# Kernel optimization log

Measured on AMD Instinct MI355X. Metric: run time of the kernel, lower is better.

## Reference

```python
import jax, jax.numpy as jnp
import numpy as np


def _sage_layer(x, src, dst, W_self, W_neigh, b, n_nodes):
    # mean aggregation over incoming edges: agg[v] = mean(x[u] for (u,v) in E)
    agg = jax.ops.segment_sum(x[src], dst, num_segments=n_nodes)          # [N, D]
    cnt = jax.ops.segment_sum(jnp.ones((src.shape[0],), x.dtype), dst,
                              num_segments=n_nodes)                        # [N]
    agg = agg / jnp.clip(cnt, 1.0)[:, None]
    # h = ReLU(x W_self^T + agg W_neigh^T + b)   (torch Linear weight is [out, in])
    h = jnp.einsum('nd,od->no', x, W_self) + jnp.einsum('nd,od->no', agg, W_neigh) + b
    return jax.nn.relu(h)


def setup_inputs() -> dict:
    key = jax.random.key(0)
    ks = jax.random.split(key, 7)
    N, E = 50000, 800000
    F_IN, H, F_OUT = 128, 256, 128
    x = jax.random.normal(ks[0], (N, F_IN), dtype=jnp.float32)
    edge_index = jax.random.randint(ks[1], (2, E), 0, N, dtype=jnp.int64)
    s = 0.05
    return {
        'x': x,
        'edge_index': edge_index,
        'W_self1': jax.random.normal(ks[2], (H, F_IN), dtype=jnp.float32) * s,
        'W_neigh1': jax.random.normal(ks[3], (H, F_IN), dtype=jnp.float32) * s,
        'b1': jnp.zeros((H,), dtype=jnp.float32),
        'W_self2': jax.random.normal(ks[4], (F_OUT, H), dtype=jnp.float32) * s,
        'W_neigh2': jax.random.normal(ks[5], (F_OUT, H), dtype=jnp.float32) * s,
        'b2': jnp.zeros((F_OUT,), dtype=jnp.float32),
    }


def reference(x, edge_index, W_self1, W_neigh1, b1, W_self2, W_neigh2, b2):
    n_nodes = x.shape[0]
    src, dst = edge_index[0], edge_index[1]
    h = _sage_layer(x, src, dst, W_self1, W_neigh1, b1, n_nodes)
    # dropout is identity at inference
    h = _sage_layer(h, src, dst, W_self2, W_neigh2, b2, n_nodes)
    return h
```

## Files before the change

kernel.cpp:

```cpp
#include <hip/hip_runtime.h>


#define CAP 64
#define CPAD 16
#define NSLICE 8

typedef __attribute__((ext_vector_type(8))) short bfrag;
typedef __attribute__((ext_vector_type(4))) float ffrag;

__device__ inline unsigned short f2bf(float f) {
    union { float f; unsigned u; } v; v.f = f;
    unsigned r = (v.u + 0x7FFFu + ((v.u >> 16) & 1u)) >> 16;
    return (unsigned short)r;
}

__global__ __launch_bounds__(256) void prep_kernel(
        const int* __restrict__ src, const int* __restrict__ dst,
        int* __restrict__ cnt, unsigned short* __restrict__ adj,
        int E, int nper, int nfill,
        const float* __restrict__ x, unsigned short* __restrict__ xb, long xn4,
        int xblocks,
        const float* __restrict__ W0, const float* __restrict__ W1,
        const float* __restrict__ W2, const float* __restrict__ W3,
        unsigned short* __restrict__ O0, unsigned short* __restrict__ O1,
        unsigned short* __restrict__ O2, unsigned short* __restrict__ O3)
{
    int b = blockIdx.x;
    if (b < nfill) {
        int slice = b & (NSLICE - 1);
        int e = (b >> 3) * 256 + (int)threadIdx.x;
        if (e >= E) return;
        int d = dst[e];
        if ((unsigned)(d - slice * nper) >= (unsigned)nper) return;
        int r = atomicAdd(&cnt[d * CPAD], 1);
        if (r < CAP) adj[(size_t)d * CAP + r] = (unsigned short)src[e];
        return;
    }
    b -= nfill;
    if (b < xblocks) {
        long i = (long)b * 256 + threadIdx.x;
        if (i >= xn4) return;
        float4 v = *(const float4*)(x + i * 4);
        ushort4 o;
        o.x = f2bf(v.x); o.y = f2bf(v.y); o.z = f2bf(v.z); o.w = f2bf(v.w);
        *(ushort4*)(xb + i * 4) = o;
        return;
    }
    b -= xblocks;
    int i = b * 256 + (int)threadIdx.x;
    int sel = i >> 13, off = i & 8191;
    const float* srcw = (sel == 0) ? W0 : (sel == 1) ? W1 : (sel == 2) ? W2 : W3;
    unsigned short* dstw = (sel == 0) ? O0 : (sel == 1) ? O1 : (sel == 2) ? O2 : O3;
    float4 v = ((const float4*)srcw)[off];
    ushort4 o;
    o.x = f2bf(v.x); o.y = f2bf(v.y); o.z = f2bf(v.z); o.w = f2bf(v.w);
    ((ushort4*)dstw)[off] = o;
}

#define BFLO(u) __uint_as_float((u) << 16)
#define BFHI(u) __uint_as_float((u) & 0xFFFF0000u)

__global__ __launch_bounds__(256) void gather_mean_bf16(
        const unsigned short* __restrict__ Xb, const int* __restrict__ cnt,
        const unsigned short* __restrict__ adj,
        unsigned short* __restrict__ aggb, int N) {
    int w = (blockIdx.x * 256 + threadIdx.x) >> 6;
    int lane = threadIdx.x & 63;
    int node = w * 2 + (lane >> 5);
    int sl = lane & 31;
    if (node >= N) return;
    int c = cnt[node * CPAD]; if (c > CAP) c = CAP;
    const unsigned short* al = adj + (size_t)node * CAP;
    float a0 = 0.f, a1 = 0.f, a2 = 0.f, a3 = 0.f;
    int j = 0;
    for (; j + 3 < c; j += 4) {
        int s0 = al[j], s1 = al[j + 1], s2 = al[j + 2], s3 = al[j + 3];
        uint2 v0 = *(const uint2*)(Xb + (size_t)s0 * 128 + sl * 4);
        uint2 v1 = *(const uint2*)(Xb + (size_t)s1 * 128 + sl * 4);
        uint2 v2 = *(const uint2*)(Xb + (size_t)s2 * 128 + sl * 4);
        uint2 v3 = *(const uint2*)(Xb + (size_t)s3 * 128 + sl * 4);
        a0 += (BFLO(v0.x) + BFLO(v1.x)) + (BFLO(v2.x) + BFLO(v3.x));
        a1 += (BFHI(v0.x) + BFHI(v1.x)) + (BFHI(v2.x) + BFHI(v3.x));
        a2 += (BFLO(v0.y) + BFLO(v1.y)) + (BFLO(v2.y) + BFLO(v3.y));
        a3 += (BFHI(v0.y) + BFHI(v1.y)) + (BFHI(v2.y) + BFHI(v3.y));
    }
    for (; j < c; ++j) {
        uint2 v = *(const uint2*)(Xb + (size_t)al[j] * 128 + sl * 4);
        a0 += BFLO(v.x); a1 += BFHI(v.x);
        a2 += BFLO(v.y); a3 += BFHI(v.y);
    }
    float s = (c > 0) ? 1.0f / (float)c : 0.0f;
    uint2 o;
    o.x = (unsigned)f2bf(a0 * s) | ((unsigned)f2bf(a1 * s) << 16);
    o.y = (unsigned)f2bf(a2 * s) | ((unsigned)f2bf(a3 * s) << 16);
    *(uint2*)(aggb + (size_t)node * 128 + sl * 4) = o;
}

__global__ __launch_bounds__(256) void gather_epilogue_bf16(
        const unsigned short* __restrict__ Zb, const unsigned short* __restrict__ S2b,
        const int* __restrict__ cnt, const unsigned short* __restrict__ adj,
        float* __restrict__ out, int N) {
    int w = (blockIdx.x * 256 + threadIdx.x) >> 6;
    int lane = threadIdx.x & 63;
    int node = w * 2 + (lane >> 5);
    int sl = lane & 31;
    if (node >= N) return;
    int c = cnt[node * CPAD]; if (c > CAP) c = CAP;
    const unsigned short* al = adj + (size_t)node * CAP;
    float a0 = 0.f, a1 = 0.f, a2 = 0.f, a3 = 0.f;
    int j = 0;
    for (; j + 3 < c; j += 4) {
        int s0 = al[j], s1 = al[j + 1], s2 = al[j + 2], s3 = al[j + 3];
        uint2 v0 = *(const uint2*)(Zb + (size_t)s0 * 128 + sl * 4);
        uint2 v1 = *(const uint2*)(Zb + (size_t)s1 * 128 + sl * 4);
        uint2 v2 = *(const uint2*)(Zb + (size_t)s2 * 128 + sl * 4);
        uint2 v3 = *(const uint2*)(Zb + (size_t)s3 * 128 + sl * 4);
        a0 += (BFLO(v0.x) + BFLO(v1.x)) + (BFLO(v2.x) + BFLO(v3.x));
        a1 += (BFHI(v0.x) + BFHI(v1.x)) + (BFHI(v2.x) + BFHI(v3.x));
        a2 += (BFLO(v0.y) + BFLO(v1.y)) + (BFLO(v2.y) + BFLO(v3.y));
        a3 += (BFHI(v0.y) + BFHI(v1.y)) + (BFHI(v2.y) + BFHI(v3.y));
    }
    for (; j < c; ++j) {
        uint2 v = *(const uint2*)(Zb + (size_t)al[j] * 128 + sl * 4);
        a0 += BFLO(v.x); a1 += BFHI(v.x);
        a2 += BFLO(v.y); a3 += BFHI(v.y);
    }
    float s = (c > 0) ? 1.0f / (float)c : 0.0f;
    uint2 sv = *(const uint2*)(S2b + (size_t)node * 128 + sl * 4);
    float4 o;
    o.x = fmaxf(BFLO(sv.x) + a0 * s, 0.0f);
    o.y = fmaxf(BFHI(sv.x) + a1 * s, 0.0f);
    o.z = fmaxf(BFLO(sv.y) + a2 * s, 0.0f);
    o.w = fmaxf(BFHI(sv.y) + a3 * s, 0.0f);
    *(float4*)(out + (size_t)node * 128 + sl * 4) = o;
}

#define L1_LOAD(NF, NTV) do {                                                  \
    const short* xr_ = xb   + (size_t)((NTV) * 16 + ln) * 128 + lk * 8;        \
    const short* ar_ = aggb + (size_t)((NTV) * 16 + ln) * 128 + lk * 8;        \
    _Pragma("unroll") for (int kc = 0; kc < 4; ++kc) {                         \
        NF[kc]     = *(const bfrag*)(xr_ + kc * 32);                           \
        NF[4 + kc] = *(const bfrag*)(ar_ + kc * 32); }                         \
} while (0)

#define L1_STEP(NF, CURNT) do {                                                \
    const int node_ = (CURNT) * 16 + ln;                                       \
    ffrag acc_[4];                                                             \
    _Pragma("unroll") for (int m = 0; m < 4; ++m) {                            \
        acc_[m][0] = bv[m].x; acc_[m][1] = bv[m].y;                            \
        acc_[m][2] = bv[m].z; acc_[m][3] = bv[m].w; }                          \
    _Pragma("unroll") for (int m = 0; m < 4; ++m) {                            \
        _Pragma("unroll") for (int kc = 0; kc < 4; ++kc)                       \
            acc_[m] = __builtin_amdgcn_mfma_f32_16x16x32_bf16(                 \
                wfs[m][kc], NF[kc], acc_[m], 0, 0, 0);                         \
        _Pragma("unroll") for (int kc = 0; kc < 4; ++kc)                       \
            acc_[m] = __builtin_amdgcn_mfma_f32_16x16x32_bf16(                 \
                wfn[m][kc], NF[4 + kc], acc_[m], 0, 0, 0); }                   \
    _Pragma("unroll") for (int m = 0; m < 4; ++m) {                            \
        ushort4 o_;                                                            \
        o_.x = f2bf(fmaxf(acc_[m][0], 0.f)); o_.y = f2bf(fmaxf(acc_[m][1], 0.f)); \
        o_.z = f2bf(fmaxf(acc_[m][2], 0.f)); o_.w = f2bf(fmaxf(acc_[m][3], 0.f)); \
        *(ushort4*)(h1b + (size_t)node_ * 256 + (wave * 4 + m) * 16 + lk * 4) = o_; } \
} while (0)

__global__ __launch_bounds__(256) void mfma_layer1(
        const short* __restrict__ xb, const short* __restrict__ aggb,
        const short* __restrict__ Ws, const short* __restrict__ Wn,
        const float* __restrict__ bias, unsigned short* __restrict__ h1b, int NT)
{
    const int wave = threadIdx.x >> 6, lane = threadIdx.x & 63;
    const int ln = lane & 15, lk = lane >> 4;

    bfrag wfs[4][4], wfn[4][4];
    #pragma unroll
    for (int m = 0; m < 4; ++m) {
        const short* ws = Ws + (size_t)((wave * 4 + m) * 16 + ln) * 128 + lk * 8;
        const short* wn = Wn + (size_t)((wave * 4 + m) * 16 + ln) * 128 + lk * 8;
        #pragma unroll
        for (int kc = 0; kc < 4; ++kc) {
            wfs[m][kc] = *(const bfrag*)(ws + kc * 32);
            wfn[m][kc] = *(const bfrag*)(wn + kc * 32);
        }
    }
    float4 bv[4];
    #pragma unroll
    for (int m = 0; m < 4; ++m)
        bv[m] = *(const float4*)(bias + (wave * 4 + m) * 16 + lk * 4);

    bfrag nfA[8], nfB[8];
    const int stride = gridDim.x;
    int nt = blockIdx.x;
    if (nt >= NT) return;
    L1_LOAD(nfA, nt);
    while (true) {
        int ntn = nt + stride;
        if (ntn < NT) L1_LOAD(nfB, ntn);
        L1_STEP(nfA, nt);
        nt = ntn; if (nt >= NT) break;
        ntn = nt + stride;
        if (ntn < NT) L1_LOAD(nfA, ntn);
        L1_STEP(nfB, nt);
        nt = ntn; if (nt >= NT) break;
    }
}

#define L2_LOAD(NF, NTV) do {                                                  \
    const short* hr_ = h1b + (size_t)((NTV) * 16 + ln) * 256 + lk * 8;         \
    _Pragma("unroll") for (int kc = 0; kc < 8; ++kc)                           \
        NF[kc] = *(const bfrag*)(hr_ + kc * 32);                               \
} while (0)

#define L2_STEP(NF, CURNT) do {                                                \
    const int node_ = (CURNT) * 16 + ln;                                       \
    ffrag aS_[2], aZ_[2];                                                      \
    _Pragma("unroll") for (int m = 0; m < 2; ++m) {                            \
        aS_[m][0] = bv[m].x; aS_[m][1] = bv[m].y;                              \
        aS_[m][2] = bv[m].z; aS_[m][3] = bv[m].w;                              \
        aZ_[m][0] = 0.f; aZ_[m][1] = 0.f; aZ_[m][2] = 0.f; aZ_[m][3] = 0.f; }  \
    _Pragma("unroll") for (int m = 0; m < 2; ++m)                              \
        _Pragma("unroll") for (int kc = 0; kc < 8; ++kc) {                     \
            aS_[m] = __builtin_amdgcn_mfma_f32_16x16x32_bf16(                  \
                wfs[m][kc], NF[kc], aS_[m], 0, 0, 0);                          \
            aZ_[m] = __builtin_amdgcn_mfma_f32_16x16x32_bf16(                  \
                wfn[m][kc], NF[kc], aZ_[m], 0, 0, 0); }                        \
    _Pragma("unroll") for (int m = 0; m < 2; ++m) {                            \
        ushort4 so_;                                                           \
        so_.x = f2bf(aS_[m][0]); so_.y = f2bf(aS_[m][1]);                      \
        so_.z = f2bf(aS_[m][2]); so_.w = f2bf(aS_[m][3]);                      \
        *(ushort4*)(s2b + (size_t)node_ * 128 + (wave * 2 + m) * 16 + lk * 4) = so_; \
        ushort4 zo_;                                                           \
        zo_.x = f2bf(aZ_[m][0]); zo_.y = f2bf(aZ_[m][1]);                      \
        zo_.z = f2bf(aZ_[m][2]); zo_.w = f2bf(aZ_[m][3]);                      \
        *(ushort4*)(z2b + (size_t)node_ * 128 + (wave * 2 + m) * 16 + lk * 4) = zo_; } \
} while (0)

__global__ __launch_bounds__(256) void mfma_layer2(
        const short* __restrict__ h1b, const short* __restrict__ Ws,
        const short* __restrict__ Wn, const float* __restrict__ bias,
        unsigned short* __restrict__ s2b, unsigned short* __restrict__ z2b, int NT)
{
    const int wave = threadIdx.x >> 6, lane = threadIdx.x & 63;
    const int ln = lane & 15, lk = lane >> 4;

    bfrag wfs[2][8], wfn[2][8];
    #pragma unroll
    for (int m = 0; m < 2; ++m) {
        const short* ws = Ws + (size_t)((wave * 2 + m) * 16 + ln) * 256 + lk * 8;
        const short* wn = Wn + (size_t)((wave * 2 + m) * 16 + ln) * 256 + lk * 8;
        #pragma unroll
        for (int kc = 0; kc < 8; ++kc) {
            wfs[m][kc] = *(const bfrag*)(ws + kc * 32);
            wfn[m][kc] = *(const bfrag*)(wn + kc * 32);
        }
    }
    float4 bv[2];
    #pragma unroll
    for (int m = 0; m < 2; ++m)
        bv[m] = *(const float4*)(bias + (wave * 2 + m) * 16 + lk * 4);

    bfrag nfA[8], nfB[8];
    const int stride = gridDim.x;
    int nt = blockIdx.x;
    if (nt >= NT) return;
    L2_LOAD(nfA, nt);
    while (true) {
        int ntn = nt + stride;
        if (ntn < NT) L2_LOAD(nfB, ntn);
        L2_STEP(nfA, nt);
        nt = ntn; if (nt >= NT) break;
        ntn = nt + stride;
        if (ntn < NT) L2_LOAD(nfA, ntn);
        L2_STEP(nfB, nt);
        nt = ntn; if (nt >= NT) break;
    }
}

extern "C" void kernel_launch(void* const* d_in, const int* in_sizes, int n_in,
                              void* d_out, int out_size, void* d_ws, size_t ws_size,
                              hipStream_t stream) {
    const float* x   = (const float*)d_in[0];
    const int*   ei  = (const int*)d_in[1];
    const float* Ws1 = (const float*)d_in[2];
    const float* Wn1 = (const float*)d_in[3];
    const float* b1  = (const float*)d_in[4];
    const float* Ws2 = (const float*)d_in[5];
    const float* Wn2 = (const float*)d_in[6];
    const float* b2  = (const float*)d_in[7];
    float* out = (float*)d_out;

    const int N = in_sizes[0] / 128;
    const int E = in_sizes[1] / 2;
    const int NT = N / 16;
    const int* src = ei;
    const int* dst = ei + E;

    unsigned short* xb   = (unsigned short*)d_ws;
    unsigned short* h1b  = xb   + (size_t)N * 128;
    unsigned short* aggb = h1b  + (size_t)N * 256;
    unsigned short* z2b  = aggb + (size_t)N * 128;
    unsigned short* s2b  = z2b  + (size_t)N * 128;
    unsigned short* Wsb1 = s2b  + (size_t)N * 128;
    unsigned short* Wnb1 = Wsb1 + 32768;
    unsigned short* Wsb2 = Wnb1 + 32768;
    unsigned short* Wnb2 = Wsb2 + 32768;
    int* cnt = (int*)(Wnb2 + 32768);
    unsigned short* adj = (unsigned short*)(cnt + (size_t)N * CPAD);

    const int nper   = (N + NSLICE - 1) / NSLICE;
    const int nfill  = ((E + 255) / 256) * NSLICE;
    const long xn4   = (long)N * 128 / 4;
    const int xblocks = (int)((xn4 + 255) / 256);
    const int prep_blocks = nfill + xblocks + 128;

    hipMemsetAsync(cnt, 0, (size_t)N * CPAD * sizeof(int), stream);
    prep_kernel<<<prep_blocks, 256, 0, stream>>>(
        src, dst, cnt, adj, E, nper, nfill,
        x, xb, xn4, xblocks,
        Ws1, Wn1, Ws2, Wn2, Wsb1, Wnb1, Wsb2, Wnb2);

    const int gather_blocks = (N * 32 + 255) / 256;

    gather_mean_bf16<<<gather_blocks, 256, 0, stream>>>(xb, cnt, adj, aggb, N);
    mfma_layer1<<<512, 256, 0, stream>>>(
        (const short*)xb, (const short*)aggb, (const short*)Wsb1, (const short*)Wnb1,
        b1, h1b, NT);

    mfma_layer2<<<512, 256, 0, stream>>>(
        (const short*)h1b, (const short*)Wsb2, (const short*)Wnb2, b2, s2b, z2b, NT);
    gather_epilogue_bf16<<<gather_blocks, 256, 0, stream>>>(
        z2b, s2b, cnt, adj, out, N);
}
```

Before: 238.3 us.

## Bucket edges by destination slice before adjacency fill; widen gather loads

Adjacency construction becomes two passes. The first pass reads each edge once and uses wave-ballot-aggregated atomics to append packed (dst,src) pairs into per-slice, per-segment buffers. The second pass then does the per-node atomic fill from those buffers. This replaces the previous scheme, where eight block copies each re-read the whole edge list and filtered by slice, so edge reads and wasted threads should drop, at the cost of an extra launch and extra buffer traffic. The gather kernels also switch to 16 lanes per node with 16-byte loads and a vectorized neighbor-index read, which cuts instruction count per gathered row.

```diff
diff --git a/kernel.cpp b/kernel.cpp
--- a/kernel.cpp
+++ b/kernel.cpp
@@ -4,6 +4,8 @@
 #define CAP 64
 #define CPAD 16
 #define NSLICE 8
+#define NSEG 4
+#define SEGCAP 32768
 
 typedef __attribute__((ext_vector_type(8))) short bfrag;
 typedef __attribute__((ext_vector_type(4))) float ffrag;
@@ -14,10 +16,10 @@
     return (unsigned short)r;
 }
 
-__global__ __launch_bounds__(256) void prep_kernel(
+__global__ __launch_bounds__(256) void prep_a(
         const int* __restrict__ src, const int* __restrict__ dst,
-        int* __restrict__ cnt, unsigned short* __restrict__ adj,
-        int E, int nper, int nfill,
+        int* __restrict__ gcount, unsigned* __restrict__ slicebuf,
+        int E, int nper, int nfillA,
         const float* __restrict__ x, unsigned short* __restrict__ xb, long xn4,
         int xblocks,
         const float* __restrict__ W0, const float* __restrict__ W1,
@@ -26,17 +28,34 @@
         unsigned short* __restrict__ O2, unsigned short* __restrict__ O3)
 {
     int b = blockIdx.x;
-    if (b < nfill) {
-        int slice = b & (NSLICE - 1);
-        int e = (b >> 3) * 256 + (int)threadIdx.x;
-        if (e >= E) return;
-        int d = dst[e];
-        if ((unsigned)(d - slice * nper) >= (unsigned)nper) return;
-        int r = atomicAdd(&cnt[d * CPAD], 1);
-        if (r < CAP) adj[(size_t)d * CAP + r] = (unsigned short)src[e];
+    if (b < nfillA) {
+        int e = b * 256 + (int)threadIdx.x;
+        int lane = threadIdx.x & 63;
+        int wid4 = ((b * 4) + (int)(threadIdx.x >> 6)) & (NSEG - 1);
+        bool valid = e < E;
+        int d = 0, s = 0;
+        if (valid) { d = dst[e]; s = src[e]; }
+        int slice = (int)((unsigned)d / (unsigned)nper);
+        #pragma unroll
+        for (int sl = 0; sl < NSLICE; ++sl) {
+            unsigned long long m = __ballot(valid && (slice == sl));
+            if (!m) continue;
+            int leader = __ffsll(m) - 1;
+            int cw = __popcll(m);
+            int base = 0;
+            if (lane == leader)
+                base = atomicAdd(&gcount[(sl * NSEG + wid4) * 16], cw);
+            base = __shfl(base, leader);
+            if (valid && (slice == sl)) {
+                int pos = base + __popcll(m & ((1ull << lane) - 1ull));
+                if (pos < SEGCAP)
+                    slicebuf[(size_t)(sl * NSEG + wid4) * SEGCAP + pos] =
+                        ((unsigned)d << 16) | (unsigned)s;
+            }
+        }
         return;
     }
-    b -= nfill;
+    b -= nfillA;
     if (b < xblocks) {
         long i = (long)b * 256 + threadIdx.x;
         if (i >= xn4) return;
@@ -57,8 +76,31 @@
     ((ushort4*)dstw)[off] = o;
 }
 
+__global__ __launch_bounds__(256) void prep_b(
+        const unsigned* __restrict__ slicebuf, const int* __restrict__ gcount,
+        int* __restrict__ cnt, unsigned short* __restrict__ adj)
+{
+    int slice = blockIdx.x & (NSLICE - 1);
+    int seg   = (blockIdx.x >> 3) & (NSEG - 1);
+    int chunk = blockIdx.x >> 5;
+    int n = gcount[(slice * NSEG + seg) * 16];
+    if (n > SEGCAP) n = SEGCAP;
+    const unsigned* sb = slicebuf + (size_t)(slice * NSEG + seg) * SEGCAP;
+    for (int i = chunk * 256 + (int)threadIdx.x; i < n; i += 16 * 256) {
+        unsigned v = sb[i];
+        int d = (int)(v >> 16), s = (int)(v & 0xFFFFu);
+        int r = atomicAdd(&cnt[d * CPAD], 1);
+        if (r < CAP) adj[(size_t)d * CAP + r] = (unsigned short)s;
+    }
+}
+
 #define BFLO(u) __uint_as_float((u) << 16)
 #define BFHI(u) __uint_as_float((u) & 0xFFFF0000u)
+
+#define ACC8(V)  do {                                                          \
+    acc0 += BFLO(V.x); acc1 += BFHI(V.x); acc2 += BFLO(V.y); acc3 += BFHI(V.y);\
+    acc4 += BFLO(V.z); acc5 += BFHI(V.z); acc6 += BFLO(V.w); acc7 += BFHI(V.w);\
+} while (0)
 
 __global__ __launch_bounds__(256) void gather_mean_bf16(
         const unsigned short* __restrict__ Xb, const int* __restrict__ cnt,
@@ -66,34 +108,33 @@
         unsigned short* __restrict__ aggb, int N) {
     int w = (blockIdx.x * 256 + threadIdx.x) >> 6;
     int lane = threadIdx.x & 63;
-    int node = w * 2 + (lane >> 5);
-    int sl = lane & 31;
+    int node = w * 4 + (lane >> 4);
+    int sl = lane & 15;
     if (node >= N) return;
     int c = cnt[node * CPAD]; if (c > CAP) c = CAP;
     const unsigned short* al = adj + (size_t)node * CAP;
-    float a0 = 0.f, a1 = 0.f, a2 = 0.f, a3 = 0.f;
+    float acc0 = 0.f, acc1 = 0.f, acc2 = 0.f, acc3 = 0.f;
+    float acc4 = 0.f, acc5 = 0.f, acc6 = 0.f, acc7 = 0.f;
     int j = 0;
     for (; j + 3 < c; j += 4) {
-        int s0 = al[j], s1 = al[j + 1], s2 = al[j + 2], s3 = al[j + 3];
-        uint2 v0 = *(const uint2*)(Xb + (size_t)s0 * 128 + sl * 4);
-        uint2 v1 = *(const uint2*)(Xb + (size_t)s1 * 128 + sl * 4);
-        uint2 v2 = *(const uint2*)(Xb + (size_t)s2 * 128 + sl * 4);
-        uint2 v3 = *(const uint2*)(Xb + (size_t)s3 * 128 + sl * 4);
-        a0 += (BFLO(v0.x) + BFLO(v1.x)) + (BFLO(v2.x) + BFLO(v3.x));
-        a1 += (BFHI(v0.x) + BFHI(v1.x)) + (BFHI(v2.x) + BFHI(v3.x));
-        a2 += (BFLO(v0.y) + BFLO(v1.y)) + (BFLO(v2.y) + BFLO(v3.y));
-        a3 += (BFHI(v0.y) + BFHI(v1.y)) + (BFHI(v2.y) + BFHI(v3.y));
+        ushort4 q = *(const ushort4*)(al + j);
+        uint4 v0 = *(const uint4*)(Xb + (size_t)q.x * 128 + sl * 8);
+        uint4 v1 = *(const uint4*)(Xb + (size_t)q.y * 128 + sl * 8);
+        uint4 v2 = *(const uint4*)(Xb + (size_t)q.z * 128 + sl * 8);
+        uint4 v3 = *(const uint4*)(Xb + (size_t)q.w * 128 + sl * 8);
+        ACC8(v0); ACC8(v1); ACC8(v2); ACC8(v3);
     }
     for (; j < c; ++j) {
-        uint2 v = *(const uint2*)(Xb + (size_t)al[j] * 128 + sl * 4);
-        a0 += BFLO(v.x); a1 += BFHI(v.x);
-        a2 += BFLO(v.y); a3 += BFHI(v.y);
+        uint4 v = *(const uint4*)(Xb + (size_t)al[j] * 128 + sl * 8);
+        ACC8(v);
     }
     float s = (c > 0) ? 1.0f / (float)c : 0.0f;
-    uint2 o;
-    o.x = (unsigned)f2bf(a0 * s) | ((unsigned)f2bf(a1 * s) << 16);
-    o.y = (unsigned)f2bf(a2 * s) | ((unsigned)f2bf(a3 * s) << 16);
-    *(uint2*)(aggb + (size_t)node * 128 + sl * 4) = o;
+    uint4 o;
+    o.x = (unsigned)f2bf(acc0 * s) | ((unsigned)f2bf(acc1 * s) << 16);
+    o.y = (unsigned)f2bf(acc2 * s) | ((unsigned)f2bf(acc3 * s) << 16);
+    o.z = (unsigned)f2bf(acc4 * s) | ((unsigned)f2bf(acc5 * s) << 16);
+    o.w = (unsigned)f2bf(acc6 * s) | ((unsigned)f2bf(acc7 * s) << 16);
+    *(uint4*)(aggb + (size_t)node * 128 + sl * 8) = o;
 }
 
 __global__ __launch_bounds__(256) void gather_epilogue_bf16(
@@ -102,37 +143,40 @@
         float* __restrict__ out, int N) {
     int w = (blockIdx.x * 256 + threadIdx.x) >> 6;
     int lane = threadIdx.x & 63;
-    int node = w * 2 + (lane >> 5);
-    int sl = lane & 31;
+    int node = w * 4 + (lane >> 4);
+    int sl = lane & 15;
     if (node >= N) return;
     int c = cnt[node * CPAD]; if (c > CAP) c = CAP;
     const unsigned short* al = adj + (size_t)node * CAP;
-    float a0 = 0.f, a1 = 0.f, a2 = 0.f, a3 = 0.f;
+    float acc0 = 0.f, acc1 = 0.f, acc2 = 0.f, acc3 = 0.f;
+    float acc4 = 0.f, acc5 = 0.f, acc6 = 0.f, acc7 = 0.f;
     int j = 0;
     for (; j + 3 < c; j += 4) {
-        int s0 = al[j], s1 = al[j + 1], s2 = al[j + 2], s3 = al[j + 3];
-        uint2 v0 = *(const uint2*)(Zb + (size_t)s0 * 128 + sl * 4);
-        uint2 v1 = *(const uint2*)(Zb + (size_t)s1 * 128 + sl * 4);
-        uint2 v2 = *(const uint2*)(Zb + (size_t)s2 * 128 + sl * 4);
-        uint2 v3 = *(const uint2*)(Zb + (size_t)s3 * 128 + sl * 4);
-        a0 += (BFLO(v0.x) + BFLO(v1.x)) + (BFLO(v2.x) + BFLO(v3.x));
-        a1 += (BFHI(v0.x) + BFHI(v1.x)) + (BFHI(v2.x) + BFHI(v3.x));
-        a2 += (BFLO(v0.y) + BFLO(v1.y)) + (BFLO(v2.y) + BFLO(v3.y));
-        a3 += (BFHI(v0.y) + BFHI(v1.y)) + (BFHI(v2.y) + BFHI(v3.y));
+        ushort4 q = *(const ushort4*)(al + j);
+        uint4 v0 = *(const uint4*)(Zb + (size_t)q.x * 128 + sl * 8);
+        uint4 v1 = *(const uint4*)(Zb + (size_t)q.y * 128 + sl * 8);
+        uint4 v2 = *(const uint4*)(Zb + (size_t)q.z * 128 + sl * 8);
+        uint4 v3 = *(const uint4*)(Zb + (size_t)q.w * 128 + sl * 8);
+        ACC8(v0); ACC8(v1); ACC8(v2); ACC8(v3);
     }
     for (; j < c; ++j) {
-        uint2 v = *(const uint2*)(Zb + (size_t)al[j] * 128 + sl * 4);
-        a0 += BFLO(v.x); a1 += BFHI(v.x);
-        a2 += BFLO(v.y); a3 += BFHI(v.y);
+        uint4 v = *(const uint4*)(Zb + (size_t)al[j] * 128 + sl * 8);
+        ACC8(v);
     }
     float s = (c > 0) ? 1.0f / (float)c : 0.0f;
-    uint2 sv = *(const uint2*)(S2b + (size_t)node * 128 + sl * 4);
-    float4 o;
-    o.x = fmaxf(BFLO(sv.x) + a0 * s, 0.0f);
-    o.y = fmaxf(BFHI(sv.x) + a1 * s, 0.0f);
-    o.z = fmaxf(BFLO(sv.y) + a2 * s, 0.0f);
-    o.w = fmaxf(BFHI(sv.y) + a3 * s, 0.0f);
-    *(float4*)(out + (size_t)node * 128 + sl * 4) = o;
+    uint4 sv = *(const uint4*)(S2b + (size_t)node * 128 + sl * 8);
+    float4 oa, ob;
+    oa.x = fmaxf(BFLO(sv.x) + acc0 * s, 0.0f);
+    oa.y = fmaxf(BFHI(sv.x) + acc1 * s, 0.0f);
+    oa.z = fmaxf(BFLO(sv.y) + acc2 * s, 0.0f);
+    oa.w = fmaxf(BFHI(sv.y) + acc3 * s, 0.0f);
+    ob.x = fmaxf(BFLO(sv.z) + acc4 * s, 0.0f);
+    ob.y = fmaxf(BFHI(sv.z) + acc5 * s, 0.0f);
+    ob.z = fmaxf(BFLO(sv.w) + acc6 * s, 0.0f);
+    ob.w = fmaxf(BFHI(sv.w) + acc7 * s, 0.0f);
+    float* op = out + (size_t)node * 128 + sl * 8;
+    *(float4*)op = oa;
+    *(float4*)(op + 4) = ob;
 }
 
 #define L1_LOAD(NF, NTV) do {                                                  \
@@ -303,22 +347,27 @@
     unsigned short* Wnb1 = Wsb1 + 32768;
     unsigned short* Wsb2 = Wnb1 + 32768;
     unsigned short* Wnb2 = Wsb2 + 32768;
-    int* cnt = (int*)(Wnb2 + 32768);
-    unsigned short* adj = (unsigned short*)(cnt + (size_t)N * CPAD);
-
-    const int nper   = (N + NSLICE - 1) / NSLICE;
-    const int nfill  = ((E + 255) / 256) * NSLICE;
-    const long xn4   = (long)N * 128 / 4;
+    int* cnt    = (int*)(Wnb2 + 32768);
+    int* gcount = cnt + (size_t)N * CPAD;
+    unsigned short* adj = (unsigned short*)(gcount + 32 * 16);
+    unsigned* slicebuf  = (unsigned*)(adj + (size_t)N * CAP);
+
+    const int nper    = (N + NSLICE - 1) / NSLICE;
+    const int nfillA  = (E + 255) / 256;
+    const long xn4    = (long)N * 128 / 4;
     const int xblocks = (int)((xn4 + 255) / 256);
-    const int prep_blocks = nfill + xblocks + 128;
-
-    hipMemsetAsync(cnt, 0, (size_t)N * CPAD * sizeof(int), stream);
-    prep_kernel<<<prep_blocks, 256, 0, stream>>>(
-        src, dst, cnt, adj, E, nper, nfill,
+    const int prep_blocks = nfillA + xblocks + 128;
+
+    hipMemsetAsync(cnt, 0, ((size_t)N * CPAD + 32 * 16) * sizeof(int), stream);
+
+    prep_a<<<prep_blocks, 256, 0, stream>>>(
+        src, dst, gcount, slicebuf, E, nper, nfillA,
         x, xb, xn4, xblocks,
         Ws1, Wn1, Ws2, Wn2, Wsb1, Wnb1, Wsb2, Wnb2);
 
-    const int gather_blocks = (N * 32 + 255) / 256;
+    prep_b<<<512, 256, 0, stream>>>(slicebuf, gcount, cnt, adj);
+
+    const int gather_blocks = (N * 16 + 255) / 256;
 
     gather_mean_bf16<<<gather_blocks, 256, 0, stream>>>(xb, cnt, adj, aggb, N);
     mfma_layer1<<<512, 256, 0, stream>>>(
```

Result: slower. 333.8 us (+40.1%).
